# Kernel tuning notes

Hardware: AMD Instinct MI355X
Metric: run time of the kernel (lower is better)

Reference implementation:

```python
import jax, jax.numpy as jnp
import numpy as np

WS = 7      # window size
SHIFT = 3   # shift size
NH = 6      # num heads
C = 192     # channels
HH = 56
WW = 56
B = 32


def _rel_coords():
    ch, cw = np.meshgrid(np.arange(WS), np.arange(WS), indexing='ij')
    coords = np.stack([ch, cw]).reshape(2, -1)            # (2, 49)
    rel = coords[:, :, None] - coords[:, None, :]          # (2, 49, 49)
    rel[0] += WS - 1
    rel[1] += WS - 1
    rel[0] *= 2 * WS - 1
    return rel.sum(0)                                      # (49, 49)


def _swin_attn_mask(Hp, Wp):
    img = np.zeros((Hp, Wp), np.int32)
    cnt = 0
    for hs in (slice(0, -WS), slice(-WS, -SHIFT), slice(-SHIFT, None)):
        for ws_ in (slice(0, -WS), slice(-WS, -SHIFT), slice(-SHIFT, None)):
            img[hs, ws_] = cnt
            cnt += 1
    win = img.reshape(Hp // WS, WS, Wp // WS, WS).transpose(0, 2, 1, 3).reshape(-1, WS * WS)
    return win[:, :, None] != win[:, None, :]              # (Nw, 49, 49) bool


def setup_inputs() -> dict:
    key = jax.random.key(0)
    ks = jax.random.split(key, 8)
    s = 0.02
    return {
        'x': jax.random.normal(ks[0], (B, HH * WW, C), jnp.float32),
        'H': HH,
        'W': WW,
        'attn_mask': jnp.asarray(_swin_attn_mask(HH, WW)),
        'relative_coords': jnp.asarray(_rel_coords(), jnp.int32),
        'norm1_w': jnp.ones((C,), jnp.float32),
        'norm1_b': jnp.zeros((C,), jnp.float32),
        'qkv_w': jax.random.normal(ks[1], (3 * C, C), jnp.float32) * s,
        'rel_bias': jax.random.normal(ks[2], ((2 * WS - 1) ** 2, NH), jnp.float32) * 0.2,
        'proj_w': jax.random.normal(ks[3], (C, C), jnp.float32) * s,
        'proj_b': jnp.zeros((C,), jnp.float32),
        'norm2_w': jnp.ones((C,), jnp.float32),
        'norm2_b': jnp.zeros((C,), jnp.float32),
        'fc1_w': jax.random.normal(ks[4], (4 * C, C), jnp.float32) * s,
        'fc1_b': jnp.zeros((4 * C,), jnp.float32),
        'fc2_w': jax.random.normal(ks[5], (C, 4 * C), jnp.float32) * s,
        'fc2_b': jnp.zeros((C,), jnp.float32),
    }


def _ln(t, w, b):
    m = t.mean(-1, keepdims=True)
    v = t.var(-1, keepdims=True)
    return (t - m) / jnp.sqrt(v + 1e-5) * w + b


def reference(x, H, W, attn_mask, relative_coords, norm1_w, norm1_b, qkv_w, rel_bias,
              proj_w, proj_b, norm2_w, norm2_b, fc1_w, fc1_b, fc2_w, fc2_b):
    Bb, L, Cd = x.shape
    nh, hd = NH, C // NH
    shortcut = x
    h = _ln(x, norm1_w, norm1_b).reshape(Bb, H, W, Cd)
    pad_h = (WS - H % WS) % WS
    pad_w = (WS - W % WS) % WS
    if pad_h or pad_w:
        h = jnp.pad(h, ((0, 0), (0, pad_h), (0, pad_w), (0, 0)))
    Hp, Wp = H + pad_h, W + pad_w
    if SHIFT > 0:
        h = jnp.roll(h, (-SHIFT, -SHIFT), axis=(1, 2))
    nWh, nWw = Hp // WS, Wp // WS
    Lw = WS * WS
    win = h.reshape(Bb, nWh, WS, nWw, WS, Cd).transpose(0, 1, 3, 2, 4, 5).reshape(-1, Lw, Cd)
    B_ = win.shape[0]
    qkv = (win @ qkv_w.T).reshape(B_, Lw, 3, nh, hd).transpose(2, 0, 3, 1, 4)
    q, k, v = qkv[0], qkv[1], qkv[2]
    # NOTE: source multiplies by num_dim**0.5 (faithful quirk)
    attn = jnp.einsum('bhid,bhjd->bhij', q, k) * (Cd ** 0.5)
    bias = rel_bias[relative_coords].transpose(2, 0, 1)    # (nh, Lw, Lw)
    attn = attn + bias[None]
    if SHIFT > 0:
        Nw = attn_mask.shape[0]
        attn = attn.reshape(-1, Nw, nh, Lw, Lw)
        attn = jnp.where(attn_mask[None, :, None], -100.0, attn)
        attn = attn.reshape(B_, nh, Lw, Lw)
    attn = jax.nn.softmax(attn, axis=-1)
    out = jnp.einsum('bhij,bhjd->bhid', attn, v).transpose(0, 2, 1, 3).reshape(B_, Lw, Cd)
    out = out @ proj_w.T + proj_b
    out = out.reshape(Bb, nWh, nWw, WS, WS, Cd).transpose(0, 1, 3, 2, 4, 5).reshape(Bb, Hp, Wp, Cd)
    if SHIFT > 0:
        out = jnp.roll(out, (SHIFT, SHIFT), axis=(1, 2))
    out = out[:, :H, :W].reshape(Bb, L, Cd)
    x = shortcut + out
    h2 = _ln(x, norm2_w, norm2_b)
    h2 = jax.nn.gelu(h2 @ fc1_w.T + fc1_b, approximate=False)
    # source MLP applies GELU (drop2 = act_layer()) after fc2 (faithful quirk)
    h2 = jax.nn.gelu(h2 @ fc2_w.T + fc2_b, approximate=False)
    return x + h2
```

## Files before the change

### kernel.cpp

```cpp
#include <hip/hip_runtime.h>

#define WS7    7
#define SHIFT3 3
#define NHEAD  6
#define CCH    192
#define HDIM   32
#define HH56   56
#define LTOK   (HH56*HH56)
#define NWIN   64
#define NBATCH 32
#define NWTOT  (NBATCH*NWIN)
#define LW     49
#define MTOK   (NWTOT*LW)

typedef unsigned short u16;
typedef unsigned int   u32;
typedef __bf16 b16;
typedef b16   b16x8 __attribute__((ext_vector_type(8)));
typedef u16   u16x8 __attribute__((ext_vector_type(8)));
typedef float f32x4 __attribute__((ext_vector_type(4)));

__device__ __forceinline__ float b2f(u16 u) {
    u32 x = ((u32)u) << 16;
    return __builtin_bit_cast(float, x);
}
__device__ __forceinline__ u16 f2b(float f) {
    u32 x = __builtin_bit_cast(u32, f);
    u32 r = x + 0x7FFFu + ((x >> 16) & 1u);
    return (u16)(r >> 16);
}
__device__ __forceinline__ float gelu_exact(float x) {
    return 0.5f * x * (1.0f + erff(x * 0.7071067811865475f));
}

__device__ __forceinline__ int map_token(int m, int &b) {
    int widx = m / LW, p = m - widx * LW;
    b = widx >> 6;
    int wloc = widx & 63;
    int wh = wloc >> 3, ww = wloc & 7;
    int i = p / WS7, j = p - i * WS7;
    int gh = wh * WS7 + i + SHIFT3; if (gh >= HH56) gh -= HH56;
    int gw = ww * WS7 + j + SHIFT3; if (gw >= HH56) gw -= HH56;
    return gh * HH56 + gw;
}

__global__ __launch_bounds__(1024) void probe_kernel(const u16* __restrict__ x, int* flag) {
    __shared__ int ch, cz;
    if (threadIdx.x == 0) { ch = 0; cz = 0; }
    __syncthreads();
    int i = threadIdx.x * 16;
    u16x8 a = *(const u16x8*)(x + i);
    u16x8 b = *(const u16x8*)(x + i + 8);
    int h = 0, z = 0;
    #pragma unroll
    for (int q = 0; q < 8; q++) {
        h += (((a[q] >> 7) & 0xFF) >= 0xC0) + (((b[q] >> 7) & 0xFF) >= 0xC0);
        z += (a[q] == 0) + (b[q] == 0);
    }
    #pragma unroll
    for (int off = 32; off > 0; off >>= 1) {
        h += __shfl_xor(h, off, 64);
        z += __shfl_xor(z, off, 64);
    }
    if ((threadIdx.x & 63) == 0) { atomicAdd(&ch, h); atomicAdd(&cz, z); }
    __syncthreads();
    if (threadIdx.x == 0) *flag = (ch > 250 || cz > 2048) ? 1 : 0;
}

#define CANON_TOTAL 445302
__global__ __launch_bounds__(256) void canon_all_kernel(
    const int* __restrict__ flag,
    const void* s0, const void* s1, const void* s2,  const void* s3,
    const void* s4, const void* s5, const void* s6,  const void* s7,
    const void* s8, const void* s9, const void* s10, const void* s11,
    char* __restrict__ ws)
{
    int i = blockIdx.x * 256 + threadIdx.x;
    if (i >= CANON_TOTAL) return;
    const void* srcs[12] = {s0, s1, s2, s3, s4, s5, s6, s7, s8, s9, s10, s11};
    const int cnt[12] = {110592, 36864, 147456, 147456, 192, 192, 192, 192, 192, 768, 192, 1014};
    const int off[12] = {64, 221248, 294976, 589888, 884800, 885184, 885568, 885952, 886336, 886720, 888256, 888640};
    int seg = 0, base = 0;
    while (seg < 11 && i >= base + cnt[seg]) { base += cnt[seg]; seg++; }
    int j = i - base;
    const void* sp = srcs[seg];
    u16* dp = (u16*)(ws + off[seg]);
    dp[j] = (*flag) ? f2b(((const float*)sp)[j]) : ((const u16*)sp)[j];
}

template<int GATHER>
__global__ __launch_bounds__(256) void ln_kernel(
    const void* __restrict__ src, const u16* __restrict__ w, const u16* __restrict__ bia,
    u16* __restrict__ dst, int m_base, const int* __restrict__ flag)
{
    int wave = threadIdx.x >> 6, lane = threadIdx.x & 63;
    int mloc = blockIdx.x * 4 + wave;
    size_t row;
    if (GATHER) { int b; int l = map_token(m_base + mloc, b); row = (size_t)b * LTOK + l; }
    else row = mloc;
    float v0, v1, v2;
    if (GATHER && *flag) {
        const float* xp = (const float*)src + row * CCH;
        v0 = xp[lane]; v1 = xp[lane + 64]; v2 = xp[lane + 128];
    } else {
        const u16* xp = (const u16*)src + row * CCH;
        v0 = b2f(xp[lane]); v1 = b2f(xp[lane + 64]); v2 = b2f(xp[lane + 128]);
    }
    float s = v0 + v1 + v2, sq = v0 * v0 + v1 * v1 + v2 * v2;
    for (int off = 32; off > 0; off >>= 1) {
        s  += __shfl_xor(s, off, 64);
        sq += __shfl_xor(sq, off, 64);
    }
    float mean = s * (1.f / 192.f);
    float var  = fmaxf(sq * (1.f / 192.f) - mean * mean, 0.f);
    float rstd = rsqrtf(var + 1e-5f);
    u16* op = dst + (size_t)mloc * CCH;
    op[lane]       = f2b((v0 - mean) * rstd * b2f(w[lane])       + b2f(bia[lane]));
    op[lane + 64]  = f2b((v1 - mean) * rstd * b2f(w[lane + 64])  + b2f(bia[lane + 64]));
    op[lane + 128] = f2b((v2 - mean) * rstd * b2f(w[lane + 128]) + b2f(bia[lane + 128]));
}

template<int ROWS>
__device__ __forceinline__ void stageL(const u16* __restrict__ g, int ldk, u16* s, int tid) {
    constexpr int ITER = ROWS * 4 / 256;
    #pragma unroll
    for (int it = 0; it < ITER; it++) {
        int t = it * 256 + tid;
        int row = t >> 2, c = t & 3;
        int cc = c ^ ((row >> 1) & 3);
        const u16* src = g + (size_t)row * ldk + cc * 8;
        u16* dst = s + (size_t)(it * 256 + (tid & ~63)) * 8;
        __builtin_amdgcn_global_load_lds(
            (const __attribute__((address_space(1))) void*)src,
            (__attribute__((address_space(3))) void*)dst, 16, 0, 0);
    }
}

template<int MODE, int KK>
__global__ __launch_bounds__(256, 3) void gemm_t(
    const u16* __restrict__ A, const u16* __restrict__ Bm,
    const u16* __restrict__ bias,
    u16* __restrict__ Cb, u16* __restrict__ X1, const void* __restrict__ Xin,
    void* __restrict__ Oout, size_t o_off, int m_base,
    const int* __restrict__ flag)
{
    __shared__ __align__(16) u16 As[2][128 * 32];
    __shared__ __align__(16) u16 Bs[2][192 * 32];
    int tid = threadIdx.x;
    int m0 = blockIdx.x * 128, n0 = blockIdx.y * 192;
    int wave = tid >> 6, lane = tid & 63;
    int wm = wave >> 1, wn = wave & 1;
    int quad = lane >> 4, mr = lane & 15;

    const u16* Ag = A + (size_t)m0 * KK;
    const u16* Bg = Bm + (size_t)n0 * KK;

    stageL<128>(Ag, KK, As[0], tid);
    stageL<192>(Bg, KK, Bs[0], tid);

    f32x4 acc[4][6] = {};
    constexpr int NSTEP = KK / 32;

    #pragma unroll 1
    for (int t = 0; t < NSTEP; t++) {
        int cur = t & 1;
        if (t + 1 < NSTEP) {
            stageL<128>(Ag + (t + 1) * 32, KK, As[cur ^ 1], tid);
            stageL<192>(Bg + (t + 1) * 32, KK, Bs[cur ^ 1], tid);
            asm volatile("s_waitcnt vmcnt(5)");
        } else {
            asm volatile("s_waitcnt vmcnt(0)");
        }
        __builtin_amdgcn_s_barrier();
        __builtin_amdgcn_sched_barrier(0);
        b16x8 a[4], b[6];
        #pragma unroll
        for (int sm = 0; sm < 4; sm++) {
            int row = wm * 64 + sm * 16 + mr;
            a[sm] = __builtin_bit_cast(b16x8,
                *(const u16x8*)&As[cur][row * 32 + (quad ^ ((row >> 1) & 3)) * 8]);
        }
        #pragma unroll
        for (int sn = 0; sn < 6; sn++) {
            int row = wn * 96 + sn * 16 + mr;
            b[sn] = __builtin_bit_cast(b16x8,
                *(const u16x8*)&Bs[cur][row * 32 + (quad ^ ((row >> 1) & 3)) * 8]);
        }
        #pragma unroll
        for (int sm = 0; sm < 4; sm++)
            #pragma unroll
            for (int sn = 0; sn < 6; sn++)
                acc[sm][sn] = __builtin_amdgcn_mfma_f32_16x16x32_bf16(a[sm], b[sn], acc[sm][sn], 0, 0, 0);
        __builtin_amdgcn_sched_barrier(0);
        __builtin_amdgcn_s_barrier();
    }

    int isf = *flag;
    #pragma unroll
    for (int sm = 0; sm < 4; sm++) {
        #pragma unroll
        for (int r = 0; r < 4; r++) {
            int mm = m0 + wm * 64 + sm * 16 + quad * 4 + r;
            int bimg = 0, limg = 0;
            if (MODE == 1) { limg = map_token(m_base + mm, bimg); }
            #pragma unroll
            for (int sn = 0; sn < 6; sn++) {
                float val = acc[sm][sn][r];
                int nn = n0 + wn * 96 + sn * 16 + mr;
                if (MODE == 0) {
                    Cb[(size_t)mm * 576 + nn] = f2b(val);
                } else if (MODE == 1) {
                    val += b2f(bias[nn]);
                    size_t idx = ((size_t)bimg * LTOK + limg) * CCH + nn;
                    float xi = isf ? ((const float*)Xin)[idx] : b2f(((const u16*)Xin)[idx]);
                    X1[idx] = f2b(xi + val);
                } else if (MODE == 2) {
                    val = gelu_exact(val + b2f(bias[nn]));
                    Cb[(size_t)mm * 768 + nn] = f2b(val);
                } else {
                    val = gelu_exact(val + b2f(bias[nn]));
                    size_t idx = (size_t)mm * CCH + nn;
                    float r2 = val + b2f(X1[idx]);
                    if (isf) ((float*)Oout)[o_off + idx] = r2;
                    else     ((u16*)Oout)[o_off + idx]  = f2b(r2);
                }
            }
        }
    }
}

__global__ __launch_bounds__(256) void attn_kernel(
    const u16* __restrict__ qkv, const u16* __restrict__ rel_bias,
    u16* __restrict__ aout)
{
    __shared__ __align__(16) u16 qs[64 * 32];
    __shared__ __align__(16) u16 ks[64 * 32];
    __shared__ __align__(16) u16 vsT[32 * 72];
    __shared__ __align__(16) u16 ps[64 * 72];
    __shared__ float bias_s[169];
    int blk = blockIdx.x;
    int widx = blk / NHEAD, head = blk - widx * NHEAD;
    int wloc = widx & 63;
    int wh = wloc >> 3, ww = wloc & 7;
    int tid = threadIdx.x;
    const u16* base = qkv + (size_t)widx * LW * 576 + head * HDIM;

    if (tid < 196) {
        int i = tid >> 2, c8 = (tid & 3) * 8;
        *(uint4*)&qs[i * 32 + c8] = *(const uint4*)(base + (size_t)i * 576 + c8);
        *(uint4*)&ks[i * 32 + c8] = *(const uint4*)(base + (size_t)i * 576 + 192 + c8);
        u16x8 vv = *(const u16x8*)(base + (size_t)i * 576 + 384 + c8);
        #pragma unroll
        for (int q = 0; q < 8; q++) vsT[(c8 + q) * 72 + i] = vv[q];
    }
    for (int idx = tid; idx < 32 * 15; idx += 256) {
        int d = idx / 15, j = 49 + (idx - d * 15);
        vsT[d * 72 + j] = 0;
    }
    if (tid < 169) bias_s[tid] = b2f(rel_bias[tid * NHEAD + head]);
    __syncthreads();

    int wave = tid >> 6, lane = tid & 63;
    int quad = lane >> 4, c = lane & 15;

    b16x8 aq = __builtin_bit_cast(b16x8, *(const u16x8*)&qs[(wave * 16 + c) * 32 + quad * 8]);
    f32x4 sacc[4];
    #pragma unroll
    for (int nt = 0; nt < 4; nt++) {
        b16x8 bk = __builtin_bit_cast(b16x8, *(const u16x8*)&ks[(nt * 16 + c) * 32 + quad * 8]);
        f32x4 z = {};
        sacc[nt] = __builtin_amdgcn_mfma_f32_16x16x32_bf16(aq, bk, z, 0, 0, 0);
    }

    const float SCALE = 13.856406460551018f;
    float val[4][4];
    int rbase = wave * 16 + quad * 4;
    #pragma unroll
    for (int r = 0; r < 4; r++) {
        int i = rbase + r;
        int ih = i / WS7, iw = i - ih * WS7;
        int ri = (wh == 7 ? (ih < 4 ? 1 : 2) : 0) * 3 + (ww == 7 ? (iw < 4 ? 1 : 2) : 0);
        #pragma unroll
        for (int nt = 0; nt < 4; nt++) {
            int j = nt * 16 + c;
            float v;
            if (i >= LW) v = 0.f;
            else if (j >= LW) v = -1e30f;
            else {
                int jh = j / WS7, jw = j - jh * WS7;
                int rj = (wh == 7 ? (jh < 4 ? 1 : 2) : 0) * 3 + (ww == 7 ? (jw < 4 ? 1 : 2) : 0);
                if (ri != rj) v = -100.0f;
                else v = fmaf(sacc[nt][r], SCALE, bias_s[(ih - jh + 6) * 13 + (iw - jw + 6)]);
            }
            val[r][nt] = v;
        }
    }

    #pragma unroll
    for (int r = 0; r < 4; r++) {
        float mx = fmaxf(fmaxf(val[r][0], val[r][1]), fmaxf(val[r][2], val[r][3]));
        for (int d = 1; d < 16; d <<= 1) mx = fmaxf(mx, __shfl_xor(mx, d, 64));
        float sum = 0.f;
        #pragma unroll
        for (int nt = 0; nt < 4; nt++) { float e = expf(val[r][nt] - mx); val[r][nt] = e; sum += e; }
        for (int d = 1; d < 16; d <<= 1) sum += __shfl_xor(sum, d, 64);
        float inv = 1.f / sum;
        int i = rbase + r;
        #pragma unroll
        for (int nt = 0; nt < 4; nt++)
            ps[i * 72 + nt * 16 + c] = f2b(val[r][nt] * inv);
    }

    f32x4 oacc[2] = {{}, {}};
    #pragma unroll
    for (int kh = 0; kh < 2; kh++) {
        b16x8 ap = __builtin_bit_cast(b16x8, *(const u16x8*)&ps[(wave * 16 + c) * 72 + kh * 32 + quad * 8]);
        #pragma unroll
        for (int nt = 0; nt < 2; nt++) {
            b16x8 bv = __builtin_bit_cast(b16x8, *(const u16x8*)&vsT[(nt * 16 + c) * 72 + kh * 32 + quad * 8]);
            oacc[nt] = __builtin_amdgcn_mfma_f32_16x16x32_bf16(ap, bv, oacc[nt], 0, 0, 0);
        }
    }
    #pragma unroll
    for (int nt = 0; nt < 2; nt++) {
        #pragma unroll
        for (int r = 0; r < 4; r++) {
            int i = rbase + r;
            if (i < LW)
                aout[((size_t)widx * LW + i) * CCH + head * HDIM + nt * 16 + c] = f2b(oacc[nt][r]);
        }
    }
}

extern "C" void kernel_launch(void* const* d_in, const int* in_sizes, int n_in,
                              void* d_out, int out_size, void* d_ws, size_t ws_size,
                              hipStream_t stream)
{
    const void* x_in = d_in[0];
    char* ws = (char*)d_ws;
    int* flag = (int*)ws;

    u16* qkvw_c  = (u16*)(ws + 64);
    u16* projw_c = (u16*)(ws + 221248);
    u16* fc1w_c  = (u16*)(ws + 294976);
    u16* fc2w_c  = (u16*)(ws + 589888);
    u16* n1w_c   = (u16*)(ws + 884800);
    u16* n1b_c   = (u16*)(ws + 885184);
    u16* n2w_c   = (u16*)(ws + 885568);
    u16* n2b_c   = (u16*)(ws + 885952);
    u16* projb_c = (u16*)(ws + 886336);
    u16* fc1b_c  = (u16*)(ws + 886720);
    u16* fc2b_c  = (u16*)(ws + 888256);
    u16* relb_c  = (u16*)(ws + 888640);

    const size_t P0 = 1u << 20;
    const size_t X1SZ   = (size_t)MTOK * CCH * 2;
    const size_t QKVSZ  = (size_t)MTOK * 576 * 2;

    u16* x1 = (u16*)(ws + P0);

    probe_kernel<<<1, 1024, 0, stream>>>((const u16*)x_in, flag);
    canon_all_kernel<<<(CANON_TOTAL + 255) / 256, 256, 0, stream>>>(
        flag,
        d_in[7], d_in[9], d_in[13], d_in[15],
        d_in[5], d_in[6], d_in[11], d_in[12],
        d_in[10], d_in[14], d_in[16], d_in[8],
        ws);

    if (ws_size >= P0 + 3 * X1SZ + QKVSZ) {
        u16* winq = (u16*)(ws + P0 + X1SZ);
        u16* aout = (u16*)(ws + P0 + 2 * X1SZ);
        u16* qkvq = (u16*)(ws + P0 + 3 * X1SZ);
        u16* h1q  = aout;

        ln_kernel<1><<<MTOK / 4, 256, 0, stream>>>(x_in, n1w_c, n1b_c, winq, 0, flag);
        gemm_t<0, 192><<<dim3(MTOK / 128, 3), 256, 0, stream>>>(
            winq, qkvw_c, nullptr, qkvq, nullptr, nullptr, nullptr, 0, 0, flag);
        attn_kernel<<<NWTOT * NHEAD, 256, 0, stream>>>(qkvq, relb_c, aout);
        gemm_t<1, 192><<<dim3(MTOK / 128, 1), 256, 0, stream>>>(
            aout, projw_c, projb_c, nullptr, x1, x_in, nullptr, 0, 0, flag);
        ln_kernel<0><<<MTOK / 4, 256, 0, stream>>>(x1, n2w_c, n2b_c, winq, 0, flag);
        gemm_t<2, 192><<<dim3(MTOK / 128, 4), 256, 0, stream>>>(
            winq, fc1w_c, fc1b_c, h1q, nullptr, nullptr, nullptr, 0, 0, flag);
        gemm_t<3, 768><<<dim3(MTOK / 128, 1), 256, 0, stream>>>(
            h1q, fc2w_c, fc2b_c, nullptr, x1, nullptr, d_out, 0, 0, flag);
    } else {
        const int QC = 8, EC = 8;
        const int MQ = MTOK / QC, ME = MTOK / EC;
        u16* winq = (u16*)(ws + P0 + X1SZ);
        u16* aout = (u16*)(ws + P0 + X1SZ + (size_t)MQ * CCH * 2);
        u16* qkvq = (u16*)(ws + P0 + X1SZ + 2 * (size_t)MQ * CCH * 2);
        u16* h1q  = winq;

        for (int q = 0; q < QC; q++) {
            int mb = q * MQ;
            ln_kernel<1><<<MQ / 4, 256, 0, stream>>>(x_in, n1w_c, n1b_c, winq, mb, flag);
            gemm_t<0, 192><<<dim3(MQ / 128, 3), 256, 0, stream>>>(
                winq, qkvw_c, nullptr, qkvq, nullptr, nullptr, nullptr, 0, mb, flag);
            attn_kernel<<<(NWTOT / QC) * NHEAD, 256, 0, stream>>>(qkvq, relb_c, aout);
            gemm_t<1, 192><<<dim3(MQ / 128, 1), 256, 0, stream>>>(
                aout, projw_c, projb_c, nullptr, x1, x_in, nullptr, 0, mb, flag);
        }
        u16* xnq = (u16*)(ws + P0 + X1SZ + (size_t)ME * 768 * 2);
        for (int e = 0; e < EC; e++) {
            size_t off = (size_t)e * ME * CCH;
            ln_kernel<0><<<ME / 4, 256, 0, stream>>>(x1 + off, n2w_c, n2b_c, xnq, 0, flag);
            gemm_t<2, 192><<<dim3(ME / 128, 4), 256, 0, stream>>>(
                xnq, fc1w_c, fc1b_c, h1q, nullptr, nullptr, nullptr, 0, 0, flag);
            gemm_t<3, 768><<<dim3(ME / 128, 1), 256, 0, stream>>>(
                h1q, fc2w_c, fc2b_c, nullptr, x1 + off, nullptr, d_out, off, 0, flag);
        }
    }
}
```

Baseline: 606.9 us.

## Fuse LayerNorm2, fc1, GELU and fc2 into one MLP kernel

```diff
diff --git a/kernel.cpp b/kernel.cpp
--- a/kernel.cpp
+++ b/kernel.cpp
@@ -120,6 +120,51 @@
     op[lane + 128] = f2b((v2 - mean) * rstd * b2f(w[lane + 128]) + b2f(bia[lane + 128]));
 }
 
+__device__ __forceinline__ void stage192(const u16* __restrict__ g, int ldg, u16* s, int tid) {
+    #pragma unroll
+    for (int it = 0; it < 7; it++) {
+        int t = it * 256 + tid;
+        if (t < 1600) {
+            int row = t / 25, c = t - row * 25;
+            int cc = (c == 24) ? 0 : c;
+            const u16* src = g + (size_t)row * ldg + cc * 8;
+            u16* dst = s + (size_t)(it * 256 + (tid & ~63)) * 8;
+            __builtin_amdgcn_global_load_lds(
+                (const __attribute__((address_space(1))) void*)src,
+                (__attribute__((address_space(3))) void*)dst, 16, 0, 0);
+        }
+    }
+}
+
+__device__ __forceinline__ void ln_lds_rows(u16* As, const u16* __restrict__ w,
+                                            const u16* __restrict__ bia, int tid) {
+    int r = tid >> 2, p = tid & 3;
+    u16* row = As + r * 200 + p * 48;
+    u16x8 vv[6];
+    float s = 0.f, sq = 0.f;
+    #pragma unroll
+    for (int j = 0; j < 6; j++) {
+        vv[j] = *(const u16x8*)(row + j * 8);
+        #pragma unroll
+        for (int q = 0; q < 8; q++) { float f = b2f(vv[j][q]); s += f; sq += f * f; }
+    }
+    s  += __shfl_xor(s, 1, 64);  s  += __shfl_xor(s, 2, 64);
+    sq += __shfl_xor(sq, 1, 64); sq += __shfl_xor(sq, 2, 64);
+    float mean = s * (1.f / 192.f);
+    float var  = fmaxf(sq * (1.f / 192.f) - mean * mean, 0.f);
+    float rstd = rsqrtf(var + 1e-5f);
+    #pragma unroll
+    for (int j = 0; j < 6; j++) {
+        u16x8 o;
+        #pragma unroll
+        for (int q = 0; q < 8; q++) {
+            int col = p * 48 + j * 8 + q;
+            o[q] = f2b((b2f(vv[j][q]) - mean) * rstd * b2f(w[col]) + b2f(bia[col]));
+        }
+        *(u16x8*)(row + j * 8) = o;
+    }
+}
+
 template<int ROWS>
 __device__ __forceinline__ void stageL(const u16* __restrict__ g, int ldk, u16* s, int tid) {
     constexpr int ITER = ROWS * 4 / 256;
@@ -209,24 +254,133 @@
                 int nn = n0 + wn * 96 + sn * 16 + mr;
                 if (MODE == 0) {
                     Cb[(size_t)mm * 576 + nn] = f2b(val);
-                } else if (MODE == 1) {
+                } else {
                     val += b2f(bias[nn]);
                     size_t idx = ((size_t)bimg * LTOK + limg) * CCH + nn;
                     float xi = isf ? ((const float*)Xin)[idx] : b2f(((const u16*)Xin)[idx]);
                     X1[idx] = f2b(xi + val);
-                } else if (MODE == 2) {
-                    val = gelu_exact(val + b2f(bias[nn]));
-                    Cb[(size_t)mm * 768 + nn] = f2b(val);
-                } else {
-                    val = gelu_exact(val + b2f(bias[nn]));
-                    size_t idx = (size_t)mm * CCH + nn;
-                    float r2 = val + b2f(X1[idx]);
-                    if (isf) ((float*)Oout)[o_off + idx] = r2;
-                    else     ((u16*)Oout)[o_off + idx]  = f2b(r2);
                 }
             }
         }
     }
+}
+
+__global__ __launch_bounds__(256, 1) void mlp_fused(
+    const u16* __restrict__ x1, const u16* __restrict__ fc1w, const u16* __restrict__ fc2w,
+    const u16* __restrict__ n2w, const u16* __restrict__ n2b,
+    const u16* __restrict__ fc1b, const u16* __restrict__ fc2b,
+    void* __restrict__ Oout, size_t o_off, const int* __restrict__ flag)
+{
+    __shared__ __align__(16) u16 Xs[128 * 200];
+    __shared__ __align__(16) u16 Hs[128 * 200];
+    __shared__ __align__(16) u16 Ws[2][192 * 32];
+    int tid = threadIdx.x;
+    int m0 = blockIdx.x * 128;
+    int wave = tid >> 6, lane = tid & 63;
+    int wm = wave >> 1, wn = wave & 1;
+    int quad = lane >> 4, mr = lane & 15;
+
+    stage192(x1 + (size_t)m0 * 192, 192, Xs, tid);
+    stage192(x1 + (size_t)(m0 + 64) * 192, 192, Xs + 64 * 200, tid);
+    stageL<192>(fc1w, 192, Ws[0], tid);
+    __syncthreads();
+    ln_lds_rows(Xs, n2w, n2b, tid);
+    ln_lds_rows(Xs + 64 * 200, n2w, n2b, tid);
+    __syncthreads();
+
+    f32x4 acc2[4][6] = {};
+    int s = 0;
+
+    #pragma unroll 1
+    for (int c = 0; c < 4; c++) {
+        f32x4 acc1[4][6] = {};
+        #pragma unroll 1
+        for (int ks = 0; ks < 6; ks++, s++) {
+            if (s + 1 < 48) {
+                int s1 = s + 1, c1 = s1 / 12, w2 = (s1 / 6) & 1, k1 = s1 % 6;
+                const u16* wp = w2 ? fc2w + c1 * 192 + k1 * 32
+                                   : fc1w + (size_t)(c1 * 192) * 192 + k1 * 32;
+                stageL<192>(wp, w2 ? 768 : 192, Ws[s1 & 1], tid);
+            }
+            b16x8 a[4], b[6];
+            #pragma unroll
+            for (int sm = 0; sm < 4; sm++) {
+                int row = wm * 64 + sm * 16 + mr;
+                a[sm] = __builtin_bit_cast(b16x8,
+                    *(const u16x8*)&Xs[row * 200 + ks * 32 + quad * 8]);
+            }
+            #pragma unroll
+            for (int sn = 0; sn < 6; sn++) {
+                int row = wn * 96 + sn * 16 + mr;
+                b[sn] = __builtin_bit_cast(b16x8,
+                    *(const u16x8*)&Ws[s & 1][row * 32 + (quad ^ ((row >> 1) & 3)) * 8]);
+            }
+            #pragma unroll
+            for (int sm = 0; sm < 4; sm++)
+                #pragma unroll
+                for (int sn = 0; sn < 6; sn++)
+                    acc1[sm][sn] = __builtin_amdgcn_mfma_f32_16x16x32_bf16(a[sm], b[sn], acc1[sm][sn], 0, 0, 0);
+            __syncthreads();
+        }
+        #pragma unroll
+        for (int sm = 0; sm < 4; sm++)
+            #pragma unroll
+            for (int sn = 0; sn < 6; sn++) {
+                int nn = wn * 96 + sn * 16 + mr;
+                float bb = b2f(fc1b[c * 192 + nn]);
+                #pragma unroll
+                for (int r = 0; r < 4; r++) {
+                    int lr = wm * 64 + sm * 16 + quad * 4 + r;
+                    Hs[lr * 200 + nn] = f2b(gelu_exact(acc1[sm][sn][r] + bb));
+                }
+            }
+        __syncthreads();
+        #pragma unroll 1
+        for (int ks = 0; ks < 6; ks++, s++) {
+            if (s + 1 < 48) {
+                int s1 = s + 1, c1 = s1 / 12, w2 = (s1 / 6) & 1, k1 = s1 % 6;
+                const u16* wp = w2 ? fc2w + c1 * 192 + k1 * 32
+                                   : fc1w + (size_t)(c1 * 192) * 192 + k1 * 32;
+                stageL<192>(wp, w2 ? 768 : 192, Ws[s1 & 1], tid);
+            }
+            b16x8 a[4], b[6];
+            #pragma unroll
+            for (int sm = 0; sm < 4; sm++) {
+                int row = wm * 64 + sm * 16 + mr;
+                a[sm] = __builtin_bit_cast(b16x8,
+                    *(const u16x8*)&Hs[row * 200 + ks * 32 + quad * 8]);
+            }
+            #pragma unroll
+            for (int sn = 0; sn < 6; sn++) {
+                int row = wn * 96 + sn * 16 + mr;
+                b[sn] = __builtin_bit_cast(b16x8,
+                    *(const u16x8*)&Ws[s & 1][row * 32 + (quad ^ ((row >> 1) & 3)) * 8]);
+            }
+            #pragma unroll
+            for (int sm = 0; sm < 4; sm++)
+                #pragma unroll
+                for (int sn = 0; sn < 6; sn++)
+                    acc2[sm][sn] = __builtin_amdgcn_mfma_f32_16x16x32_bf16(a[sm], b[sn], acc2[sm][sn], 0, 0, 0);
+            __syncthreads();
+        }
+    }
+
+    int isf = *flag;
+    #pragma unroll
+    for (int sm = 0; sm < 4; sm++)
+        #pragma unroll
+        for (int sn = 0; sn < 6; sn++) {
+            int nn = wn * 96 + sn * 16 + mr;
+            float bb = b2f(fc2b[nn]);
+            #pragma unroll
+            for (int r = 0; r < 4; r++) {
+                int mm = m0 + wm * 64 + sm * 16 + quad * 4 + r;
+                size_t idx = (size_t)mm * CCH + nn;
+                float val = gelu_exact(acc2[sm][sn][r] + bb) + b2f(x1[idx]);
+                if (isf) ((float*)Oout)[o_off + idx] = val;
+                else     ((u16*)Oout)[o_off + idx]  = f2b(val);
+            }
+        }
 }
 
 __global__ __launch_bounds__(256) void attn_kernel(
@@ -371,7 +525,6 @@
         u16* winq = (u16*)(ws + P0 + X1SZ);
         u16* aout = (u16*)(ws + P0 + 2 * X1SZ);
         u16* qkvq = (u16*)(ws + P0 + 3 * X1SZ);
-        u16* h1q  = aout;
 
         ln_kernel<1><<<MTOK / 4, 256, 0, stream>>>(x_in, n1w_c, n1b_c, winq, 0, flag);
         gemm_t<0, 192><<<dim3(MTOK / 128, 3), 256, 0, stream>>>(
@@ -379,18 +532,12 @@
         attn_kernel<<<NWTOT * NHEAD, 256, 0, stream>>>(qkvq, relb_c, aout);
         gemm_t<1, 192><<<dim3(MTOK / 128, 1), 256, 0, stream>>>(
             aout, projw_c, projb_c, nullptr, x1, x_in, nullptr, 0, 0, flag);
-        ln_kernel<0><<<MTOK / 4, 256, 0, stream>>>(x1, n2w_c, n2b_c, winq, 0, flag);
-        gemm_t<2, 192><<<dim3(MTOK / 128, 4), 256, 0, stream>>>(
-            winq, fc1w_c, fc1b_c, h1q, nullptr, nullptr, nullptr, 0, 0, flag);
-        gemm_t<3, 768><<<dim3(MTOK / 128, 1), 256, 0, stream>>>(
-            h1q, fc2w_c, fc2b_c, nullptr, x1, nullptr, d_out, 0, 0, flag);
     } else {
-        const int QC = 8, EC = 8;
-        const int MQ = MTOK / QC, ME = MTOK / EC;
+        const int QC = 8;
+        const int MQ = MTOK / QC;
         u16* winq = (u16*)(ws + P0 + X1SZ);
         u16* aout = (u16*)(ws + P0 + X1SZ + (size_t)MQ * CCH * 2);
         u16* qkvq = (u16*)(ws + P0 + X1SZ + 2 * (size_t)MQ * CCH * 2);
-        u16* h1q  = winq;
 
         for (int q = 0; q < QC; q++) {
             int mb = q * MQ;
@@ -401,14 +548,8 @@
             gemm_t<1, 192><<<dim3(MQ / 128, 1), 256, 0, stream>>>(
                 aout, projw_c, projb_c, nullptr, x1, x_in, nullptr, 0, mb, flag);
         }
-        u16* xnq = (u16*)(ws + P0 + X1SZ + (size_t)ME * 768 * 2);
-        for (int e = 0; e < EC; e++) {
-            size_t off = (size_t)e * ME * CCH;
-            ln_kernel<0><<<ME / 4, 256, 0, stream>>>(x1 + off, n2w_c, n2b_c, xnq, 0, flag);
-            gemm_t<2, 192><<<dim3(ME / 128, 4), 256, 0, stream>>>(
-                xnq, fc1w_c, fc1b_c, h1q, nullptr, nullptr, nullptr, 0, 0, flag);
-            gemm_t<3, 768><<<dim3(ME / 128, 1), 256, 0, stream>>>(
-                h1q, fc2w_c, fc2b_c, nullptr, x1 + off, nullptr, d_out, off, 0, flag);
-        }
-    }
-}
+    }
+
+    mlp_fused<<<MTOK / 128, 256, 0, stream>>>(
+        x1, fc1w_c, fc2w_c, n2w_c, n2b_c, fc1b_c, fc2b_c, d_out, 0, flag);
+}
```

New measurement: 714.0 us. 1.18x slower.
